# Kernel optimization log

Hardware: AMD Instinct MI355X
Metric: run time of the kernel (lower is better)

The kernel has to match this reference:

```python
import jax, jax.numpy as jnp
import numpy as np

NEG_SLOPE = 0.2   # PyG GATConv default leaky_relu slope
L2_EPS = 1e-12    # F.normalize eps


def setup_inputs() -> dict:
    key = jax.random.key(0)
    ks = jax.random.split(key, 10)
    N, E, d = 100000, 600000, 128
    s = 1.0 / np.sqrt(d)
    return {
        "x": jax.random.normal(ks[0], (N, d), jnp.float32),
        "edge_index": jax.random.randint(ks[1], (2, E), 0, N, jnp.int64),
        "W_gat": jax.random.normal(ks[2], (d, d), jnp.float32) * s,
        "att_src": jax.random.normal(ks[3], (d,), jnp.float32) * s,
        "att_dst": jax.random.normal(ks[4], (d,), jnp.float32) * s,
        "b_gat": jax.random.normal(ks[5], (d,), jnp.float32) * s,
        "W_l": jax.random.normal(ks[6], (d, d), jnp.float32) * s,
        "b_l": jax.random.normal(ks[7], (d,), jnp.float32) * s,
        "W_r": jax.random.normal(ks[8], (d, d), jnp.float32) * s,
    }


def reference(x, edge_index, W_gat, att_src, att_dst, b_gat, W_l, b_l, W_r):
    N = x.shape[0]
    src0, dst0 = edge_index[0], edge_index[1]

    # ---- GATConv (heads=1), add_self_loops=True, dropout skipped (eval) ----
    loop = jnp.arange(N, dtype=edge_index.dtype)
    src = jnp.concatenate([src0, loop])
    dst = jnp.concatenate([dst0, loop])

    h = x @ W_gat                           # [N, d]
    a_src = h @ att_src                     # [N]
    a_dst = h @ att_dst                     # [N]
    e = jax.nn.leaky_relu(a_src[src] + a_dst[dst], NEG_SLOPE)  # [E+N]
    # segment softmax over edges sharing the same target node
    m = jax.ops.segment_max(e, dst, num_segments=N)
    p = jnp.exp(e - m[dst])
    z = jax.ops.segment_sum(p, dst, num_segments=N)
    alpha = p / z[dst]
    h_gat = jax.ops.segment_sum(h[src] * alpha[:, None], dst, num_segments=N) + b_gat

    # ---- SAGEConv((x, x_target), edge_index), mean aggr, normalize=True ----
    agg = jax.ops.segment_sum(h_gat[src0], dst0, num_segments=N)   # [N, d]
    cnt = jax.ops.segment_sum(jnp.ones_like(src0, dtype=h_gat.dtype), dst0, num_segments=N)
    mean = agg / jnp.maximum(cnt, 1.0)[:, None]
    out = mean @ W_l + b_l + h_gat @ W_r    # x_target = h_gat[:N]
    # F.normalize(out, p=2, dim=-1)
    norm = jnp.sqrt(jnp.sum(out * out, axis=-1, keepdims=True))
    out = out / jnp.maximum(norm, L2_EPS)
    return out
```

## Files before the change

kernel.cpp:

```cpp
#include <hip/hip_runtime.h>
#include <hip/hip_bf16.h>

#define D 128
#define NEG_SLOPE 0.2f
#define SCAN_BS 512

typedef __attribute__((ext_vector_type(8))) short short8;
typedef __attribute__((ext_vector_type(4))) float f32x4;

__device__ __forceinline__ float group_max16(float v) {
#pragma unroll
    for (int m = 8; m >= 1; m >>= 1) v = fmaxf(v, __shfl_xor(v, m));
    return v;
}
__device__ __forceinline__ float group_sum16(float v) {
#pragma unroll
    for (int m = 8; m >= 1; m >>= 1) v += __shfl_xor(v, m);
    return v;
}

__device__ __forceinline__ unsigned short f2bfu(float f) {
    __hip_bfloat16 h = __float2bfloat16(f);
    return *reinterpret_cast<unsigned short*>(&h);
}

__device__ __forceinline__ float bf2f(unsigned short u) {
    return __uint_as_float(((unsigned)u) << 16);
}

__device__ __forceinline__ short8 load_bf8(const float* p) {
    float4 p0 = *(const float4*)p;
    float4 p1 = *(const float4*)(p + 4);
    short8 r;
    r[0] = (short)f2bfu(p0.x); r[1] = (short)f2bfu(p0.y);
    r[2] = (short)f2bfu(p0.z); r[3] = (short)f2bfu(p0.w);
    r[4] = (short)f2bfu(p1.x); r[5] = (short)f2bfu(p1.y);
    r[6] = (short)f2bfu(p1.z); r[7] = (short)f2bfu(p1.w);
    return r;
}

__global__ void k_wt(const float* __restrict__ Wg, const float* __restrict__ Wl,
                     const float* __restrict__ Wr, short* __restrict__ WgT,
                     short* __restrict__ WlT, short* __restrict__ WrT) {
    int i = blockIdx.x * blockDim.x + threadIdx.x;
    int m = i >> 14;
    int r = (i >> 7) & 127;
    int c = i & 127;
    const float* src = (m == 0) ? Wg : (m == 1) ? Wl : Wr;
    short* dst = (m == 0) ? WgT : (m == 1) ? WlT : WrT;
    dst[r * D + c] = (short)f2bfu(src[c * D + r]);
}

__global__ void k_hist(const int* __restrict__ ei, int* __restrict__ cnt, int E) {
    int i = blockIdx.x * blockDim.x + threadIdx.x;
    if (i < E) atomicAdd(&cnt[ei[E + i]], 1);
}

__global__ void k_scan_block(const int* __restrict__ cnt, int* __restrict__ incl,
                             int* __restrict__ btot, int N) {
    __shared__ int s[SCAN_BS];
    int t = threadIdx.x, i = blockIdx.x * SCAN_BS + t;
    int v = (i < N) ? cnt[i] : 0;
    s[t] = v;
    __syncthreads();
    for (int d = 1; d < SCAN_BS; d <<= 1) {
        int u = (t >= d) ? s[t - d] : 0;
        __syncthreads();
        s[t] += u;
        __syncthreads();
    }
    if (i < N) incl[i] = s[t];
    if (t == SCAN_BS - 1) btot[blockIdx.x] = s[t];
}

__global__ void k_scan_tot(int* __restrict__ btot, int nb) {
    __shared__ int s[1024];
    int t = threadIdx.x;
    int v = (t < nb) ? btot[t] : 0;
    s[t] = v;
    __syncthreads();
    for (int d = 1; d < 1024; d <<= 1) {
        int u = (t >= d) ? s[t - d] : 0;
        __syncthreads();
        s[t] += u;
        __syncthreads();
    }
    if (t < nb) btot[t] = s[t] - v;
}

__global__ void k_scan_add(const int* __restrict__ cnt, int* __restrict__ off,
                           const int* __restrict__ btot, int N) {
    int i = blockIdx.x * blockDim.x + threadIdx.x;
    if (i < N) off[i] = off[i] + btot[i / SCAN_BS] - cnt[i];
}

__global__ void k_bucket(const int* __restrict__ ei, const int* __restrict__ off,
                         int* __restrict__ fill, int* __restrict__ csr, int E) {
    int i = blockIdx.x * blockDim.x + threadIdx.x;
    if (i < E) {
        int dt = ei[E + i];
        int p = off[dt] + atomicAdd(&fill[dt], 1);
        csr[p] = ei[i];
    }
}

__global__ void k_gemm_h(const float* __restrict__ x, const short* __restrict__ WgT,
                         const float* __restrict__ att_src, const float* __restrict__ att_dst,
                         unsigned short* __restrict__ h_bf, float* __restrict__ a_src,
                         float* __restrict__ a_dst, int N) {
    const int lane = threadIdx.x & 63;
    const int wave = threadIdx.x >> 6;
    const int r0 = blockIdx.x * 64 + wave * 16;
    const int lrow = lane & 15, lgrp = lane >> 4;
    const int arow = r0 + lrow;
    const bool ok = (arow < N);

    short8 afr[4];
    const float* xr = x + (size_t)arow * D + lgrp * 8;
#pragma unroll
    for (int kt = 0; kt < 4; ++kt) {
        if (ok) afr[kt] = load_bf8(xr + kt * 32);
        else { short8 zf; for (int j = 0; j < 8; ++j) zf[j] = 0; afr[kt] = zf; }
    }

    f32x4 acc[8];
#pragma unroll
    for (int f = 0; f < 8; ++f) acc[f] = (f32x4){0.f, 0.f, 0.f, 0.f};
#pragma unroll
    for (int f = 0; f < 8; ++f) {
        const short* wb = WgT + ((f * 16 + lrow) * D + lgrp * 8);
#pragma unroll
        for (int kt = 0; kt < 4; ++kt) {
            short8 b = *(const short8*)(wb + kt * 32);
            acc[f] = __builtin_amdgcn_mfma_f32_16x16x32_bf16(afr[kt], b, acc[f], 0, 0, 0);
        }
    }

    float ps[4] = {0.f, 0.f, 0.f, 0.f}, pd[4] = {0.f, 0.f, 0.f, 0.f};
    const int rbase = r0 + lgrp * 4;
#pragma unroll
    for (int f = 0; f < 8; ++f) {
        int col = f * 16 + lrow;
        float as = att_src[col], ad = att_dst[col];
#pragma unroll
        for (int j = 0; j < 4; ++j) {
            float v = acc[f][j];
            if (rbase + j < N) h_bf[(size_t)(rbase + j) * D + col] = f2bfu(v);
            ps[j] += v * as;
            pd[j] += v * ad;
        }
    }
#pragma unroll
    for (int m = 8; m >= 1; m >>= 1)
#pragma unroll
        for (int j = 0; j < 4; ++j) {
            ps[j] += __shfl_xor(ps[j], m);
            pd[j] += __shfl_xor(pd[j], m);
        }
    if (lrow == 0) {
#pragma unroll
        for (int j = 0; j < 4; ++j)
            if (rbase + j < N) { a_src[rbase + j] = ps[j]; a_dst[rbase + j] = pd[j]; }
    }
}

__global__ void k_attn(const int* __restrict__ csr, const int* __restrict__ off,
                       const int* __restrict__ cnt, const float* __restrict__ a_src,
                       const float* __restrict__ a_dst, const unsigned short* __restrict__ h_bf,
                       const float* __restrict__ bg, unsigned short* __restrict__ hg_bf, int N) {
    const int lane = threadIdx.x & 63;
    const int l16 = lane & 15, grp = lane >> 4;
    const int gbase = grp << 4;
    const int d = blockIdx.x * 16 + ((threadIdx.x >> 6) << 2) + grp;
    if (d >= N) return;
    const int deg = cnt[d], o = off[d];
    const float ad = a_dst[d];
    float es = a_src[d] + ad;
    es = (es > 0.f) ? es : NEG_SLOPE * es;

    const int fo = l16 * 8;
    short8 hv = *(const short8*)(h_bf + (size_t)d * D + fo);
    float acc[8];
    float inv;

    if (deg <= 16) {
        int sv = 0;
        float e = -INFINITY;
        if (l16 < deg) {
            sv = csr[o + l16];
            float t = a_src[sv] + ad;
            e = (t > 0.f) ? t : NEG_SLOPE * t;
        }
        float mx = fmaxf(group_max16(e), es);
        float p = (l16 < deg) ? expf(e - mx) : 0.f;
        float pself = expf(es - mx);
        inv = 1.f / (group_sum16(p) + pself);
#pragma unroll
        for (int j = 0; j < 8; ++j) acc[j] = pself * bf2f((unsigned short)hv[j]);
        int i = 0;
        for (; i + 4 <= deg; i += 4) {
            int s0 = __shfl(sv, gbase + i);
            int s1 = __shfl(sv, gbase + i + 1);
            int s2 = __shfl(sv, gbase + i + 2);
            int s3 = __shfl(sv, gbase + i + 3);
            float p0 = __shfl(p, gbase + i);
            float p1 = __shfl(p, gbase + i + 1);
            float p2 = __shfl(p, gbase + i + 2);
            float p3 = __shfl(p, gbase + i + 3);
            short8 r0 = *(const short8*)(h_bf + (size_t)s0 * D + fo);
            short8 r1 = *(const short8*)(h_bf + (size_t)s1 * D + fo);
            short8 r2 = *(const short8*)(h_bf + (size_t)s2 * D + fo);
            short8 r3 = *(const short8*)(h_bf + (size_t)s3 * D + fo);
#pragma unroll
            for (int j = 0; j < 8; ++j)
                acc[j] += p0 * bf2f((unsigned short)r0[j]) + p1 * bf2f((unsigned short)r1[j])
                        + p2 * bf2f((unsigned short)r2[j]) + p3 * bf2f((unsigned short)r3[j]);
        }
        for (; i < deg; ++i) {
            int s = __shfl(sv, gbase + i);
            float pi = __shfl(p, gbase + i);
            short8 row = *(const short8*)(h_bf + (size_t)s * D + fo);
#pragma unroll
            for (int j = 0; j < 8; ++j) acc[j] += pi * bf2f((unsigned short)row[j]);
        }
    } else {
        float m2 = es;
        for (int i = l16; i < deg; i += 16) {
            float t = a_src[csr[o + i]] + ad;
            t = (t > 0.f) ? t : NEG_SLOPE * t;
            m2 = fmaxf(m2, t);
        }
        float mx = group_max16(m2);
        float zp = 0.f;
        for (int i = l16; i < deg; i += 16) {
            float t = a_src[csr[o + i]] + ad;
            t = (t > 0.f) ? t : NEG_SLOPE * t;
            zp += expf(t - mx);
        }
        float pself = expf(es - mx);
        inv = 1.f / (group_sum16(zp) + pself);
#pragma unroll
        for (int j = 0; j < 8; ++j) acc[j] = pself * bf2f((unsigned short)hv[j]);
        for (int i = 0; i < deg; ++i) {
            int s = csr[o + i];
            float t = a_src[s] + ad;
            t = (t > 0.f) ? t : NEG_SLOPE * t;
            float pi = expf(t - mx);
            short8 row = *(const short8*)(h_bf + (size_t)s * D + fo);
#pragma unroll
            for (int j = 0; j < 8; ++j) acc[j] += pi * bf2f((unsigned short)row[j]);
        }
    }
    short8 r;
#pragma unroll
    for (int j = 0; j < 8; ++j) r[j] = (short)f2bfu(acc[j] * inv + bg[fo + j]);
    *(short8*)(hg_bf + (size_t)d * D + fo) = r;
}

__global__ void k_out(const int* __restrict__ csr, const int* __restrict__ off,
                      const int* __restrict__ cnt, const unsigned short* __restrict__ hg_bf,
                      const short* __restrict__ WlT, const short* __restrict__ WrT,
                      const float* __restrict__ bl, float* __restrict__ out, int N) {
    __shared__ unsigned short lds_mean[64 * D];
    const int lane = threadIdx.x & 63;
    const int wave = threadIdx.x >> 6;
    const int r0 = blockIdx.x * 64;
    const int wr0 = wave * 16;
    const int lrow = lane & 15, lgrp = lane >> 4;
    const int arow = r0 + wr0 + lrow;
    const bool ok = (arow < N);

    short8 ah[4];
    {
        const unsigned short* hp = hg_bf + (size_t)arow * D + lgrp * 8;
#pragma unroll
        for (int kt = 0; kt < 4; ++kt) {
            if (ok) ah[kt] = *(const short8*)(hp + kt * 32);
            else { short8 zf; for (int j = 0; j < 8; ++j) zf[j] = 0; ah[kt] = zf; }
        }
    }
    f32x4 acc[8];
#pragma unroll
    for (int f = 0; f < 8; ++f) {
        float b = bl[f * 16 + lrow];
        acc[f] = (f32x4){b, b, b, b};
    }

    {
        const int l16 = lane & 15, grp = lane >> 4;
        const int gbase = grp << 4;
        const int fo = l16 * 8;
#pragma unroll
        for (int p = 0; p < 4; ++p) {
            const int lrow_ = wr0 + p * 4 + grp;
            const int d = r0 + lrow_;
            float macc[8];
#pragma unroll
            for (int j = 0; j < 8; ++j) macc[j] = 0.f;
            float minv = 0.f;
            if (d < N) {
                const int deg = cnt[d], o = off[d];
                if (deg <= 16) {
                    int sv = 0;
                    if (l16 < deg) sv = csr[o + l16];
                    int i = 0;
                    for (; i + 4 <= deg; i += 4) {
                        int s0 = __shfl(sv, gbase + i);
                        int s1 = __shfl(sv, gbase + i + 1);
                        int s2 = __shfl(sv, gbase + i + 2);
                        int s3 = __shfl(sv, gbase + i + 3);
                        short8 r0_ = *(const short8*)(hg_bf + (size_t)s0 * D + fo);
                        short8 r1_ = *(const short8*)(hg_bf + (size_t)s1 * D + fo);
                        short8 r2_ = *(const short8*)(hg_bf + (size_t)s2 * D + fo);
                        short8 r3_ = *(const short8*)(hg_bf + (size_t)s3 * D + fo);
#pragma unroll
                        for (int j = 0; j < 8; ++j)
                            macc[j] += bf2f((unsigned short)r0_[j]) + bf2f((unsigned short)r1_[j])
                                     + bf2f((unsigned short)r2_[j]) + bf2f((unsigned short)r3_[j]);
                    }
                    for (; i < deg; ++i) {
                        int s = __shfl(sv, gbase + i);
                        short8 row = *(const short8*)(hg_bf + (size_t)s * D + fo);
#pragma unroll
                        for (int j = 0; j < 8; ++j) macc[j] += bf2f((unsigned short)row[j]);
                    }
                } else {
                    for (int i = 0; i < deg; ++i) {
                        int s = csr[o + i];
                        short8 row = *(const short8*)(hg_bf + (size_t)s * D + fo);
#pragma unroll
                        for (int j = 0; j < 8; ++j) macc[j] += bf2f((unsigned short)row[j]);
                    }
                }
                minv = 1.f / fmaxf((float)deg, 1.f);
            }
            short8 r;
#pragma unroll
            for (int j = 0; j < 8; ++j) r[j] = (short)f2bfu(macc[j] * minv);
            *(short8*)(lds_mean + lrow_ * D + fo) = r;
        }
    }

    short8 am[4];
    const unsigned short* mp = lds_mean + (wr0 + lrow) * D + lgrp * 8;
#pragma unroll
    for (int kt = 0; kt < 4; ++kt) am[kt] = *(const short8*)(mp + kt * 32);

#pragma unroll
    for (int f = 0; f < 8; ++f) {
        const short* wl = WlT + ((f * 16 + lrow) * D + lgrp * 8);
        const short* wr = WrT + ((f * 16 + lrow) * D + lgrp * 8);
#pragma unroll
        for (int kt = 0; kt < 4; ++kt) {
            short8 b0 = *(const short8*)(wl + kt * 32);
            acc[f] = __builtin_amdgcn_mfma_f32_16x16x32_bf16(am[kt], b0, acc[f], 0, 0, 0);
            short8 b1 = *(const short8*)(wr + kt * 32);
            acc[f] = __builtin_amdgcn_mfma_f32_16x16x32_bf16(ah[kt], b1, acc[f], 0, 0, 0);
        }
    }

    float ss[4] = {0.f, 0.f, 0.f, 0.f};
#pragma unroll
    for (int f = 0; f < 8; ++f)
#pragma unroll
        for (int j = 0; j < 4; ++j) ss[j] += acc[f][j] * acc[f][j];
#pragma unroll
    for (int m = 8; m >= 1; m >>= 1)
#pragma unroll
        for (int j = 0; j < 4; ++j) ss[j] += __shfl_xor(ss[j], m);

    const int rbase = r0 + wr0 + lgrp * 4;
#pragma unroll
    for (int j = 0; j < 4; ++j) {
        int r = rbase + j;
        if (r < N) {
            float sc = 1.f / fmaxf(sqrtf(ss[j]), 1e-12f);
#pragma unroll
            for (int f = 0; f < 8; ++f)
                out[(size_t)r * D + f * 16 + lrow] = acc[f][j] * sc;
        }
    }
}

extern "C" void kernel_launch(void* const* d_in, const int* in_sizes, int n_in,
                              void* d_out, int out_size, void* d_ws, size_t ws_size,
                              hipStream_t stream) {
    const float* x       = (const float*)d_in[0];
    const int*   ei      = (const int*)d_in[1];
    const float* Wg      = (const float*)d_in[2];
    const float* att_src = (const float*)d_in[3];
    const float* att_dst = (const float*)d_in[4];
    const float* bg      = (const float*)d_in[5];
    const float* Wl      = (const float*)d_in[6];
    const float* bl      = (const float*)d_in[7];
    const float* Wr      = (const float*)d_in[8];
    const int N = in_sizes[0] / D;
    const int E = in_sizes[1] / 2;

    char* w = (char*)d_ws;
    unsigned short* h_bf  = (unsigned short*)w;  w += (size_t)N * D * 2;
    unsigned short* hg_bf = (unsigned short*)w;  w += (size_t)N * D * 2;
    float* a_src = (float*)w;  w += (size_t)N * 4;
    float* a_dst = (float*)w;  w += (size_t)N * 4;
    int*   cnt_i = (int*)w;    w += (size_t)N * 4;
    int*   off   = (int*)w;    w += (size_t)N * 4;
    int*   fill  = (int*)w;    w += (size_t)N * 4;
    int*   btot  = (int*)w;    w += 1024 * 4;
    int*   csr   = (int*)w;    w += (size_t)E * 4;
    short* WgT   = (short*)w;  w += (size_t)D * D * 2;
    short* WlT   = (short*)w;  w += (size_t)D * D * 2;
    short* WrT   = (short*)w;  w += (size_t)D * D * 2;
    float* out_f = (float*)d_out;

    (void)hipMemsetAsync(cnt_i, 0, (size_t)N * 4, stream);
    (void)hipMemsetAsync(fill, 0, (size_t)N * 4, stream);

    const int nb = (N + SCAN_BS - 1) / SCAN_BS;

    k_wt<<<(3 * D * D) / 256, 256, 0, stream>>>(Wg, Wl, Wr, WgT, WlT, WrT);
    k_hist<<<(E + 255) / 256, 256, 0, stream>>>(ei, cnt_i, E);
    k_scan_block<<<nb, SCAN_BS, 0, stream>>>(cnt_i, off, btot, N);
    k_scan_tot<<<1, 1024, 0, stream>>>(btot, nb);
    k_scan_add<<<(N + 255) / 256, 256, 0, stream>>>(cnt_i, off, btot, N);
    k_bucket<<<(E + 255) / 256, 256, 0, stream>>>(ei, off, fill, csr, E);

    k_gemm_h<<<(N + 63) / 64, 256, 0, stream>>>(x, WgT, att_src, att_dst, h_bf, a_src, a_dst, N);
    k_attn<<<(N + 15) / 16, 256, 0, stream>>>(csr, off, cnt_i, a_src, a_dst, h_bf, bg, hg_bf, N);
    k_out<<<(N + 63) / 64, 256, 0, stream>>>(csr, off, cnt_i, hg_bf, WlT, WrT, bl, out_f, N);
}
```

Before: 236.1 us.

## Apply SAGE linear before neighbor aggregation and split output kernel

Uses linearity of the mean aggregation to compute hg·Wl and hg·Wr+b in a dense GEMM kernel first, then gathers and averages the transformed bf16 rows in a separate kernel that adds the root term and L2-normalizes. This decouples the irregular gather from the MFMA tile so each kernel can run with better occupancy and no LDS staging. It adds an extra N×D bf16 intermediate and a read-modify-write of the fp32 output, increasing memory traffic, and rounds the transformed features to bf16 before averaging.

```diff
diff --git a/kernel.cpp b/kernel.cpp
--- a/kernel.cpp
+++ b/kernel.cpp
@@ -257,95 +257,32 @@
     *(short8*)(hg_bf + (size_t)d * D + fo) = r;
 }
 
-__global__ void k_out(const int* __restrict__ csr, const int* __restrict__ off,
-                      const int* __restrict__ cnt, const unsigned short* __restrict__ hg_bf,
-                      const short* __restrict__ WlT, const short* __restrict__ WrT,
-                      const float* __restrict__ bl, float* __restrict__ out, int N) {
-    __shared__ unsigned short lds_mean[64 * D];
+__global__ void k_gemm2(const unsigned short* __restrict__ hg_bf,
+                        const short* __restrict__ WlT, const short* __restrict__ WrT,
+                        const float* __restrict__ bl, unsigned short* __restrict__ hgWl_bf,
+                        float* __restrict__ outw, int N) {
     const int lane = threadIdx.x & 63;
     const int wave = threadIdx.x >> 6;
-    const int r0 = blockIdx.x * 64;
-    const int wr0 = wave * 16;
+    const int r0 = blockIdx.x * 64 + wave * 16;
     const int lrow = lane & 15, lgrp = lane >> 4;
-    const int arow = r0 + wr0 + lrow;
+    const int arow = r0 + lrow;
     const bool ok = (arow < N);
 
     short8 ah[4];
-    {
-        const unsigned short* hp = hg_bf + (size_t)arow * D + lgrp * 8;
-#pragma unroll
-        for (int kt = 0; kt < 4; ++kt) {
-            if (ok) ah[kt] = *(const short8*)(hp + kt * 32);
-            else { short8 zf; for (int j = 0; j < 8; ++j) zf[j] = 0; ah[kt] = zf; }
-        }
-    }
-    f32x4 acc[8];
+    const unsigned short* hp = hg_bf + (size_t)arow * D + lgrp * 8;
+#pragma unroll
+    for (int kt = 0; kt < 4; ++kt) {
+        if (ok) ah[kt] = *(const short8*)(hp + kt * 32);
+        else { short8 zf; for (int j = 0; j < 8; ++j) zf[j] = 0; ah[kt] = zf; }
+    }
+
+    f32x4 accL[8], accR[8];
 #pragma unroll
     for (int f = 0; f < 8; ++f) {
+        accL[f] = (f32x4){0.f, 0.f, 0.f, 0.f};
         float b = bl[f * 16 + lrow];
-        acc[f] = (f32x4){b, b, b, b};
-    }
-
-    {
-        const int l16 = lane & 15, grp = lane >> 4;
-        const int gbase = grp << 4;
-        const int fo = l16 * 8;
-#pragma unroll
-        for (int p = 0; p < 4; ++p) {
-            const int lrow_ = wr0 + p * 4 + grp;
-            const int d = r0 + lrow_;
-            float macc[8];
-#pragma unroll
-            for (int j = 0; j < 8; ++j) macc[j] = 0.f;
-            float minv = 0.f;
-            if (d < N) {
-                const int deg = cnt[d], o = off[d];
-                if (deg <= 16) {
-                    int sv = 0;
-                    if (l16 < deg) sv = csr[o + l16];
-                    int i = 0;
-                    for (; i + 4 <= deg; i += 4) {
-                        int s0 = __shfl(sv, gbase + i);
-                        int s1 = __shfl(sv, gbase + i + 1);
-                        int s2 = __shfl(sv, gbase + i + 2);
-                        int s3 = __shfl(sv, gbase + i + 3);
-                        short8 r0_ = *(const short8*)(hg_bf + (size_t)s0 * D + fo);
-                        short8 r1_ = *(const short8*)(hg_bf + (size_t)s1 * D + fo);
-                        short8 r2_ = *(const short8*)(hg_bf + (size_t)s2 * D + fo);
-                        short8 r3_ = *(const short8*)(hg_bf + (size_t)s3 * D + fo);
-#pragma unroll
-                        for (int j = 0; j < 8; ++j)
-                            macc[j] += bf2f((unsigned short)r0_[j]) + bf2f((unsigned short)r1_[j])
-                                     + bf2f((unsigned short)r2_[j]) + bf2f((unsigned short)r3_[j]);
-                    }
-                    for (; i < deg; ++i) {
-                        int s = __shfl(sv, gbase + i);
-                        short8 row = *(const short8*)(hg_bf + (size_t)s * D + fo);
-#pragma unroll
-                        for (int j = 0; j < 8; ++j) macc[j] += bf2f((unsigned short)row[j]);
-                    }
-                } else {
-                    for (int i = 0; i < deg; ++i) {
-                        int s = csr[o + i];
-                        short8 row = *(const short8*)(hg_bf + (size_t)s * D + fo);
-#pragma unroll
-                        for (int j = 0; j < 8; ++j) macc[j] += bf2f((unsigned short)row[j]);
-                    }
-                }
-                minv = 1.f / fmaxf((float)deg, 1.f);
-            }
-            short8 r;
-#pragma unroll
-            for (int j = 0; j < 8; ++j) r[j] = (short)f2bfu(macc[j] * minv);
-            *(short8*)(lds_mean + lrow_ * D + fo) = r;
-        }
-    }
-
-    short8 am[4];
-    const unsigned short* mp = lds_mean + (wr0 + lrow) * D + lgrp * 8;
-#pragma unroll
-    for (int kt = 0; kt < 4; ++kt) am[kt] = *(const short8*)(mp + kt * 32);
-
+        accR[f] = (f32x4){b, b, b, b};
+    }
 #pragma unroll
     for (int f = 0; f < 8; ++f) {
         const short* wl = WlT + ((f * 16 + lrow) * D + lgrp * 8);
@@ -353,33 +290,92 @@
 #pragma unroll
         for (int kt = 0; kt < 4; ++kt) {
             short8 b0 = *(const short8*)(wl + kt * 32);
-            acc[f] = __builtin_amdgcn_mfma_f32_16x16x32_bf16(am[kt], b0, acc[f], 0, 0, 0);
+            accL[f] = __builtin_amdgcn_mfma_f32_16x16x32_bf16(ah[kt], b0, accL[f], 0, 0, 0);
             short8 b1 = *(const short8*)(wr + kt * 32);
-            acc[f] = __builtin_amdgcn_mfma_f32_16x16x32_bf16(ah[kt], b1, acc[f], 0, 0, 0);
-        }
-    }
-
-    float ss[4] = {0.f, 0.f, 0.f, 0.f};
-#pragma unroll
-    for (int f = 0; f < 8; ++f)
-#pragma unroll
-        for (int j = 0; j < 4; ++j) ss[j] += acc[f][j] * acc[f][j];
-#pragma unroll
-    for (int m = 8; m >= 1; m >>= 1)
-#pragma unroll
-        for (int j = 0; j < 4; ++j) ss[j] += __shfl_xor(ss[j], m);
-
-    const int rbase = r0 + wr0 + lgrp * 4;
-#pragma unroll
-    for (int j = 0; j < 4; ++j) {
-        int r = rbase + j;
-        if (r < N) {
-            float sc = 1.f / fmaxf(sqrtf(ss[j]), 1e-12f);
-#pragma unroll
-            for (int f = 0; f < 8; ++f)
-                out[(size_t)r * D + f * 16 + lrow] = acc[f][j] * sc;
-        }
-    }
+            accR[f] = __builtin_amdgcn_mfma_f32_16x16x32_bf16(ah[kt], b1, accR[f], 0, 0, 0);
+        }
+    }
+
+    const int rbase = r0 + lgrp * 4;
+#pragma unroll
+    for (int f = 0; f < 8; ++f) {
+        int col = f * 16 + lrow;
+#pragma unroll
+        for (int j = 0; j < 4; ++j) {
+            int r = rbase + j;
+            if (r < N) {
+                hgWl_bf[(size_t)r * D + col] = f2bfu(accL[f][j]);
+                outw[(size_t)r * D + col] = accR[f][j];
+            }
+        }
+    }
+}
+
+__global__ void k_final(const int* __restrict__ csr, const int* __restrict__ off,
+                        const int* __restrict__ cnt, const unsigned short* __restrict__ hgWl_bf,
+                        float* __restrict__ outw, int N) {
+    const int lane = threadIdx.x & 63;
+    const int l16 = lane & 15, grp = lane >> 4;
+    const int gbase = grp << 4;
+    const int d = blockIdx.x * 16 + ((threadIdx.x >> 6) << 2) + grp;
+    if (d >= N) return;
+    const int deg = cnt[d], o = off[d];
+    const int fo = l16 * 8;
+
+    float acc[8];
+#pragma unroll
+    for (int j = 0; j < 8; ++j) acc[j] = 0.f;
+
+    if (deg <= 16) {
+        int sv = 0;
+        if (l16 < deg) sv = csr[o + l16];
+        int i = 0;
+        for (; i + 4 <= deg; i += 4) {
+            int s0 = __shfl(sv, gbase + i);
+            int s1 = __shfl(sv, gbase + i + 1);
+            int s2 = __shfl(sv, gbase + i + 2);
+            int s3 = __shfl(sv, gbase + i + 3);
+            short8 r0 = *(const short8*)(hgWl_bf + (size_t)s0 * D + fo);
+            short8 r1 = *(const short8*)(hgWl_bf + (size_t)s1 * D + fo);
+            short8 r2 = *(const short8*)(hgWl_bf + (size_t)s2 * D + fo);
+            short8 r3 = *(const short8*)(hgWl_bf + (size_t)s3 * D + fo);
+#pragma unroll
+            for (int j = 0; j < 8; ++j)
+                acc[j] += bf2f((unsigned short)r0[j]) + bf2f((unsigned short)r1[j])
+                        + bf2f((unsigned short)r2[j]) + bf2f((unsigned short)r3[j]);
+        }
+        for (; i < deg; ++i) {
+            int s = __shfl(sv, gbase + i);
+            short8 row = *(const short8*)(hgWl_bf + (size_t)s * D + fo);
+#pragma unroll
+            for (int j = 0; j < 8; ++j) acc[j] += bf2f((unsigned short)row[j]);
+        }
+    } else {
+        for (int i = 0; i < deg; ++i) {
+            int s = csr[o + i];
+            short8 row = *(const short8*)(hgWl_bf + (size_t)s * D + fo);
+#pragma unroll
+            for (int j = 0; j < 8; ++j) acc[j] += bf2f((unsigned short)row[j]);
+        }
+    }
+
+    const float minv = 1.f / fmaxf((float)deg, 1.f);
+    float* orow = outw + (size_t)d * D + fo;
+    float4 v0 = *(const float4*)orow;
+    float4 v1 = *(const float4*)(orow + 4);
+    float v[8] = {v0.x + acc[0] * minv, v0.y + acc[1] * minv,
+                  v0.z + acc[2] * minv, v0.w + acc[3] * minv,
+                  v1.x + acc[4] * minv, v1.y + acc[5] * minv,
+                  v1.z + acc[6] * minv, v1.w + acc[7] * minv};
+    float ss = 0.f;
+#pragma unroll
+    for (int j = 0; j < 8; ++j) ss += v[j] * v[j];
+    ss = group_sum16(ss);
+    float sc = 1.f / fmaxf(sqrtf(ss), 1e-12f);
+    float4 w0 = {v[0] * sc, v[1] * sc, v[2] * sc, v[3] * sc};
+    float4 w1 = {v[4] * sc, v[5] * sc, v[6] * sc, v[7] * sc};
+    *(float4*)orow = w0;
+    *(float4*)(orow + 4) = w1;
 }
 
 extern "C" void kernel_launch(void* const* d_in, const int* in_sizes, int n_in,
@@ -398,8 +394,9 @@
     const int E = in_sizes[1] / 2;
 
     char* w = (char*)d_ws;
-    unsigned short* h_bf  = (unsigned short*)w;  w += (size_t)N * D * 2;
-    unsigned short* hg_bf = (unsigned short*)w;  w += (size_t)N * D * 2;
+    unsigned short* h_bf    = (unsigned short*)w;  w += (size_t)N * D * 2;
+    unsigned short* hg_bf   = (unsigned short*)w;  w += (size_t)N * D * 2;
+    unsigned short* hgWl_bf = (unsigned short*)w;  w += (size_t)N * D * 2;
     float* a_src = (float*)w;  w += (size_t)N * 4;
     float* a_dst = (float*)w;  w += (size_t)N * 4;
     int*   cnt_i = (int*)w;    w += (size_t)N * 4;
@@ -426,5 +423,6 @@
 
     k_gemm_h<<<(N + 63) / 64, 256, 0, stream>>>(x, WgT, att_src, att_dst, h_bf, a_src, a_dst, N);
     k_attn<<<(N + 15) / 16, 256, 0, stream>>>(csr, off, cnt_i, a_src, a_dst, h_bf, bg, hg_bf, N);
-    k_out<<<(N + 63) / 64, 256, 0, stream>>>(csr, off, cnt_i, hg_bf, WlT, WrT, bl, out_f, N);
-}
+    k_gemm2<<<(N + 63) / 64, 256, 0, stream>>>(hg_bf, WlT, WrT, bl, hgWl_bf, out_f, N);
+    k_final<<<(N + 15) / 16, 256, 0, stream>>>(csr, off, cnt_i, hgWl_bf, out_f, N);
+}
```

Result: slower. 255.7 us (+8.3%).
